# Kernel tuning notes

Measured on AMD Instinct MI355X. Metric: run time of the kernel, lower is better.

The kernel has to match this reference:

```python
import jax, jax.numpy as jnp
import numpy as np

# ---- config (mirrors the repo-level globals) ----
B, N = 8, 1024                 # batch, points per cloud
SHAPE_SIZE = 256               # per-point shape-code width
HEAD = 8                       # point_size + 1 - shape_size passthrough channels
SC_HID = 256                   # shape_code_encoder_hidden_dims = [256]
SC_OUT = 128                   # shape_code_encoder_output_size
E = 16                         # num_categories
INTER = HEAD + SC_OUT          # 136
ENC_DIMS = [INTER, 256, 512]   # encoder_hidden_dims
LATENT = 1024                  # latent_size
DEC_DIMS = [LATENT, 1024, 2048]
MAX_PTS, PSI = 1024, 7         # max_num_points, point_size_intermediate
DEC_OUT = (PSI + 1) * MAX_PTS  # 8192


def setup_inputs() -> dict:
    key = jax.random.key(0)
    ks = jax.random.split(key, 20)
    s = 0.02
    inp = {
        'x': jax.random.normal(ks[0], (B, HEAD + SHAPE_SIZE, N), jnp.float32),
        'cats': jax.random.randint(ks[1], (B, N), 0, E),
        # per-category shape encoders: Linear(256->256) ReLU Linear(256->128)
        'W1': jax.random.normal(ks[2], (E, SHAPE_SIZE, SC_HID), jnp.float32) * s,
        'b1': jnp.zeros((E, SC_HID), jnp.float32),
        'W2': jax.random.normal(ks[3], (E, SC_HID, SC_OUT), jnp.float32) * s,
        'b2': jnp.zeros((E, SC_OUT), jnp.float32),
        # pointwise Conv1d stack 136->256->512->1024 (weights [out,in])
        'Wc1': jax.random.normal(ks[4], (ENC_DIMS[1], ENC_DIMS[0]), jnp.float32) * s,
        'bc1': jnp.zeros((ENC_DIMS[1],), jnp.float32),
        'Wc2': jax.random.normal(ks[5], (ENC_DIMS[2], ENC_DIMS[1]), jnp.float32) * s,
        'bc2': jnp.zeros((ENC_DIMS[2],), jnp.float32),
        'Wc3': jax.random.normal(ks[6], (LATENT, ENC_DIMS[2]), jnp.float32) * s,
        'bc3': jnp.zeros((LATENT,), jnp.float32),
        # decoder MLP 1024->1024->2048->8192 (weights [in,out])
        'Wd1': jax.random.normal(ks[7], (DEC_DIMS[0], DEC_DIMS[1]), jnp.float32) * s,
        'bd1': jnp.zeros((DEC_DIMS[1],), jnp.float32),
        'Wd2': jax.random.normal(ks[8], (DEC_DIMS[1], DEC_DIMS[2]), jnp.float32) * s,
        'bd2': jnp.zeros((DEC_DIMS[2],), jnp.float32),
        'Wd3': jax.random.normal(ks[9], (DEC_DIMS[2], DEC_OUT), jnp.float32) * s,
        'bd3': jnp.zeros((DEC_OUT,), jnp.float32),
    }
    return inp


def reference(x, cats, W1, b1, W2, b2, Wc1, bc1, Wc2, bc2, Wc3, bc3,
              Wd1, bd1, Wd2, bd2, Wd3, bd3):
    # ---- encoder: category-routed per-point shape MLP ----
    sf = jnp.swapaxes(x[:, -SHAPE_SIZE:, :], 1, 2)      # [B, N, 256]
    mask = jax.nn.one_hot(cats, E, dtype=x.dtype)       # [B, N, E]
    routed = jnp.zeros((B, N, SC_OUT), x.dtype)
    for e in range(E):  # fixed small expert loop; avoids [B,N,E,hid] blowup
        h = jax.nn.relu(sf @ W1[e] + b1[e])             # [B, N, 256]
        o = h @ W2[e] + b2[e]                           # [B, N, 128]
        routed = routed + mask[..., e:e + 1] * o
    xi = jnp.concatenate([x[:, :HEAD, :], jnp.swapaxes(routed, 1, 2)], axis=1)  # [B,136,N]
    # ---- pointwise conv stack + max pool ----
    h = jax.nn.relu(jnp.einsum('oc,bcn->bon', Wc1, xi) + bc1[:, None])
    h = jax.nn.relu(jnp.einsum('oc,bcn->bon', Wc2, h) + bc2[:, None])
    h = jnp.einsum('oc,bcn->bon', Wc3, h) + bc3[:, None]  # [B, 1024, N]
    latent = jnp.max(h, axis=2)                            # [B, 1024]
    # ---- decoder MLP ----
    d = jax.nn.relu(latent @ Wd1 + bd1)
    d = jax.nn.relu(d @ Wd2 + bd2)
    out = (d @ Wd3 + bd3).reshape(B, MAX_PTS, PSI + 1)     # [B, 1024, 8]
    return out, latent
```

## Files before the change

kernel.cpp:

```cpp
#include <hip/hip_runtime.h>
#include <math.h>

#define BB 8
#define NN 1024
#define HEADC 8
#define SS 256
#define SCO 128
#define NE 16
#define C1 256
#define C2 512
#define C3 1024
#define NPTS (BB*NN)
#define XCH (HEADC+SS)
#define K1P 192
#define BK 64

typedef unsigned short ushortT;
typedef __attribute__((ext_vector_type(8))) short bf16x8;
typedef __attribute__((ext_vector_type(4))) float f32x4;

#define OB_XTB    0ull
#define OB_HB     4325376ull
#define OB_H2     0ull
#define OB_XI     8519680ull
#define OB_H1     11665408ull
#define OB_WT1    15859712ull
#define OB_WT2    15958016ull
#define OB_WT3    16220160ull
#define OB_W1T    17268736ull
#define OB_W2T    19365888ull
#define OB_PMAX   20414464ull
#define OB_LAT    20676608ull
#define OB_D1     20709376ull
#define OB_D2     20742144ull
#define OB_DPARTA 20807680ull
#define OB_DPARTB 22904832ull
#define OB_DPARTC 20807680ull
#define OB_IDX    33390592ull
#define OB_OFFS   33423360ull

__device__ __forceinline__ ushortT f2b(float f) {
  unsigned u = __float_as_uint(f);
  return (ushortT)((u + 0x7FFFu + ((u >> 16) & 1u)) >> 16);
}

#define CW_S1 (256*192)
#define CW_S2 (512*256)
#define CW_S3 (1024*512)
#define PREP_P1 2304
#define PREP_P2 5056
#define PREP_P3 7104
#define PREP_GRID 7105

__global__ __launch_bounds__(256) void k_prep_all(
    const float* __restrict__ x, ushortT* __restrict__ xTb, ushortT* __restrict__ xi,
    const float* __restrict__ Wc1, const float* __restrict__ Wc2,
    const float* __restrict__ Wc3, ushortT* __restrict__ w1c,
    ushortT* __restrict__ w2c, ushortT* __restrict__ w3c,
    const float* __restrict__ W1, const float* __restrict__ W2,
    ushortT* __restrict__ W1tb, ushortT* __restrict__ W2tb,
    const int* __restrict__ cats, int* __restrict__ idx, int* __restrict__ offs) {
  __shared__ float t[32][33];
  __shared__ int cnt[NE], base[NE + 1], cur[NE];
  int bid = blockIdx.x;
  int tid = threadIdx.x;

  if (bid < PREP_P1) {
    int bx = bid & 31, by = (bid >> 5) % 9, bz = bid / 288;
    int n0 = bx * 32, c0 = by * 32;
    int tx = tid & 31, ty = tid >> 5;
    const float* s = x + (size_t)bz * XCH * NN;
    for (int yy = ty; yy < 32; yy += 8) {
      int c = c0 + yy;
      if (c < XCH) t[yy][tx] = s[(size_t)c * NN + n0 + tx];
    }
    __syncthreads();
    for (int yy = ty; yy < 32; yy += 8) {
      int n = n0 + yy, c = c0 + tx;
      if (c < XCH) {
        ushortT v = f2b(t[tx][yy]);
        xTb[(size_t)(bz * NN + n) * XCH + c] = v;
        if (c < HEADC) xi[(size_t)(bz * NN + n) * K1P + c] = v;
      }
    }
  } else if (bid < PREP_P2) {
    int i = (bid - PREP_P1) * 256 + tid;
    if (i < CW_S1) {
      int r = i / K1P, c = i - r * K1P;
      w1c[i] = (c < 136) ? f2b(Wc1[(size_t)r * 136 + c]) : (ushortT)0;
    } else if (i < CW_S1 + CW_S2) {
      int k = i - CW_S1;
      w2c[k] = f2b(Wc2[k]);
    } else if (i < CW_S1 + CW_S2 + CW_S3) {
      int k = i - CW_S1 - CW_S2;
      w3c[k] = f2b(Wc3[k]);
    }
  } else if (bid < PREP_P3) {
    int tt = bid - PREP_P2;
    int z = tt >> 6, ry = (tt >> 3) & 7, cx = tt & 7;
    const float* s;
    ushortT* d;
    int C;
    if (z < 16) { s = W1 + (size_t)z * 65536; d = W1tb + (size_t)z * 65536; C = 256; }
    else {
      if (cx >= 4) return;
      s = W2 + (size_t)(z - 16) * 32768; d = W2tb + (size_t)(z - 16) * 32768; C = 128;
    }
    int r0 = ry * 32, c0 = cx * 32;
    int tx = tid & 31, ty = tid >> 5;
    for (int yy = ty; yy < 32; yy += 8) {
      int r = r0 + yy, c = c0 + tx;
      if (c < C) t[yy][tx] = s[(size_t)r * C + c];
    }
    __syncthreads();
    for (int yy = ty; yy < 32; yy += 8) {
      int c = c0 + yy, r = r0 + tx;
      if (c < C) d[(size_t)c * 256 + r] = f2b(t[tx][yy]);
    }
  } else {
    if (tid < NE) cnt[tid] = 0;
    __syncthreads();
    for (int p = tid; p < NPTS; p += 256) atomicAdd(&cnt[cats[p]], 1);
    __syncthreads();
    if (tid == 0) {
      int s = 0;
      for (int e = 0; e < NE; ++e) { base[e] = s; cur[e] = s; s += cnt[e]; }
      base[NE] = s;
    }
    __syncthreads();
    for (int p = tid; p < NPTS; p += 256) {
      int pos = atomicAdd(&cur[cats[p]], 1);
      idx[pos] = p;
    }
    if (tid <= NE) offs[tid] = base[tid];
  }
}

template<int MODE>
__global__ __launch_bounds__(256) void k_gemm(
    const ushortT* __restrict__ A, int lda,
    const ushortT* __restrict__ Bt, int ldb,
    const float* __restrict__ bias,
    ushortT* __restrict__ Cb, int ldc,
    float* __restrict__ pmaxOut,
    const int* __restrict__ idx, const int* __restrict__ offsp,
    int K, int relu) {
  __shared__ ushortT As[128 * BK];
  __shared__ ushortT Bs[128 * BK];
  __shared__ int pts[128];
  __shared__ float smax[2][128];
  int tid = threadIdx.x;
  int wave = tid >> 6, lane = tid & 63;
  int wm = wave >> 1, wn = wave & 1;
  int g = lane >> 4, lr = lane & 15;
  int n0 = blockIdx.x * 128;
  int m0 = 0, nr = 128, bucket0 = 0;

  if constexpr (MODE == 2 || MODE == 3) {
    int e = blockIdx.y, t = blockIdx.z;
    int s0 = offsp[e];
    int cnt = offsp[e + 1] - s0;
    int p0 = t * 128;
    if (p0 >= cnt) return;
    nr = min(128, cnt - p0);
    bucket0 = s0 + p0;
    Bt += (size_t)e * ((MODE == 2) ? 256 * 256 : 128 * 256);
    bias += e * ((MODE == 2) ? 256 : 128);
    if (tid < 128) pts[tid] = (tid < nr) ? idx[bucket0 + tid] : 0;
  } else {
    m0 = blockIdx.y * 128;
  }

  f32x4 acc[4][4];
#pragma unroll
  for (int mi = 0; mi < 4; ++mi)
#pragma unroll
    for (int nj = 0; nj < 4; ++nj) acc[mi][nj] = (f32x4)(0.f);

  int nkt = K / BK;
  for (int kt = 0; kt < nkt; ++kt) {
    int k0 = kt * BK;
    __syncthreads();
#pragma unroll
    for (int i = 0; i < 4; ++i) {
      int c = tid + i * 256;
      int row = c >> 3, slot = c & 7;
      int ss = slot ^ (row & 7);
      uint4 v;
      if constexpr (MODE == 2) {
        if (row < nr) v = *(const uint4*)(A + (size_t)pts[row] * lda + 8 + k0 + slot * 8);
        else { v.x = v.y = v.z = v.w = 0u; }
      } else if constexpr (MODE == 3) {
        if (row < nr) v = *(const uint4*)(A + (size_t)(bucket0 + row) * lda + k0 + slot * 8);
        else { v.x = v.y = v.z = v.w = 0u; }
      } else {
        v = *(const uint4*)(A + (size_t)(m0 + row) * lda + k0 + slot * 8);
      }
      *(uint4*)(As + row * BK + ss * 8) = v;
      uint4 w = *(const uint4*)(Bt + (size_t)(n0 + row) * ldb + k0 + slot * 8);
      *(uint4*)(Bs + row * BK + ss * 8) = w;
    }
    __syncthreads();
#pragma unroll
    for (int kk = 0; kk < 2; ++kk) {
      bf16x8 av[4], bv[4];
#pragma unroll
      for (int mi = 0; mi < 4; ++mi) {
        int row = wm * 64 + mi * 16 + lr;
        int slot = (kk * 4 + g) ^ (row & 7);
        av[mi] = *(const bf16x8*)(As + row * BK + slot * 8);
      }
#pragma unroll
      for (int nj = 0; nj < 4; ++nj) {
        int row = wn * 64 + nj * 16 + lr;
        int slot = (kk * 4 + g) ^ (row & 7);
        bv[nj] = *(const bf16x8*)(Bs + row * BK + slot * 8);
      }
#pragma unroll
      for (int mi = 0; mi < 4; ++mi)
#pragma unroll
        for (int nj = 0; nj < 4; ++nj)
          acc[mi][nj] = __builtin_amdgcn_mfma_f32_16x16x32_bf16(av[mi], bv[nj], acc[mi][nj], 0, 0, 0);
    }
  }

  if constexpr (MODE == 1) {
#pragma unroll
    for (int nj = 0; nj < 4; ++nj) {
      float m = -INFINITY;
#pragma unroll
      for (int mi = 0; mi < 4; ++mi)
#pragma unroll
        for (int r = 0; r < 4; ++r) m = fmaxf(m, acc[mi][nj][r]);
      m = fmaxf(m, __shfl_xor(m, 16));
      m = fmaxf(m, __shfl_xor(m, 32));
      if (lane < 16) smax[wm][wn * 64 + nj * 16 + lr] = m;
    }
    __syncthreads();
    if (tid < 128) {
      float m = fmaxf(smax[0][tid], smax[1][tid]);
      pmaxOut[(size_t)blockIdx.y * C3 + n0 + tid] = m + bias[n0 + tid];
    }
  } else {
#pragma unroll
    for (int mi = 0; mi < 4; ++mi)
#pragma unroll
      for (int nj = 0; nj < 4; ++nj)
#pragma unroll
        for (int r = 0; r < 4; ++r) {
          int lrow = wm * 64 + mi * 16 + g * 4 + r;
          int col = n0 + wn * 64 + nj * 16 + lr;
          float v = acc[mi][nj][r] + bias[col];
          if (relu) v = fmaxf(v, 0.f);
          ushortT b = f2b(v);
          if constexpr (MODE == 0) {
            Cb[(size_t)(m0 + lrow) * ldc + col] = b;
          } else if constexpr (MODE == 2) {
            if (lrow < nr) Cb[(size_t)(bucket0 + lrow) * ldc + col] = b;
          } else {
            if (lrow < nr) Cb[(size_t)pts[lrow] * ldc + 8 + col] = b;
          }
        }
  }
}

__global__ __launch_bounds__(256) void k_latmax(
    const float* __restrict__ pmax, float* __restrict__ lat, float* __restrict__ outLat) {
  int id4 = blockIdx.x * 256 + threadIdx.x;
  int b = id4 >> 8, o4 = id4 & 255;
  f32x4 m = (f32x4)(-INFINITY);
  for (int t = 0; t < 8; ++t) {
    f32x4 v = *(const f32x4*)(pmax + (size_t)((b << 3) + t) * C3 + o4 * 4);
#pragma unroll
    for (int r = 0; r < 4; ++r) m[r] = fmaxf(m[r], v[r]);
  }
  *(f32x4*)(lat + (size_t)id4 * 4) = m;
  *(f32x4*)(outLat + (size_t)id4 * 4) = m;
}

template<int CHUNKLOG, int T>
__global__ __launch_bounds__(T, 1) void k_dec(
    const float* __restrict__ A, const float* __restrict__ W,
    float* __restrict__ part, int K, int N) {
  constexpr int CHUNK = 1 << CHUNKLOG;
  __shared__ float a[8 << CHUNKLOG];
  int i0 = blockIdx.y << CHUNKLOG;
  int tid = threadIdx.x;
  for (int idx = tid; idx < (8 << CHUNKLOG); idx += T)
    a[idx] = A[(size_t)(idx >> CHUNKLOG) * K + i0 + (idx & (CHUNK - 1))];
  __syncthreads();

  int col = (blockIdx.x * T + tid) * 4;
  const float* wp = W + (size_t)i0 * N + col;
  f32x4 acc[8];
#pragma unroll
  for (int r = 0; r < 8; ++r) acc[r] = (f32x4)(0.f);

  f32x4 wa[8], wb[8];
#pragma unroll
  for (int q = 0; q < 8; ++q) wa[q] = *(const f32x4*)(wp + (size_t)q * N);
#pragma unroll
  for (int q = 0; q < 8; ++q) wb[q] = *(const f32x4*)(wp + (size_t)(8 + q) * N);

  for (int k0 = 0; k0 < CHUNK; k0 += 16) {
#pragma unroll
    for (int r = 0; r < 8; ++r) {
      f32x4 av0 = *(const f32x4*)(&a[(r << CHUNKLOG) + k0]);
      f32x4 av1 = *(const f32x4*)(&a[(r << CHUNKLOG) + k0 + 4]);
      acc[r] += av0[0] * wa[0] + av0[1] * wa[1] + av0[2] * wa[2] + av0[3] * wa[3];
      acc[r] += av1[0] * wa[4] + av1[1] * wa[5] + av1[2] * wa[6] + av1[3] * wa[7];
    }
    if (k0 + 16 < CHUNK) {
#pragma unroll
      for (int q = 0; q < 8; ++q) wa[q] = *(const f32x4*)(wp + (size_t)(k0 + 16 + q) * N);
    }
#pragma unroll
    for (int r = 0; r < 8; ++r) {
      f32x4 av0 = *(const f32x4*)(&a[(r << CHUNKLOG) + k0 + 8]);
      f32x4 av1 = *(const f32x4*)(&a[(r << CHUNKLOG) + k0 + 12]);
      acc[r] += av0[0] * wb[0] + av0[1] * wb[1] + av0[2] * wb[2] + av0[3] * wb[3];
      acc[r] += av1[0] * wb[4] + av1[1] * wb[5] + av1[2] * wb[6] + av1[3] * wb[7];
    }
    if (k0 + 24 < CHUNK) {
#pragma unroll
      for (int q = 0; q < 8; ++q) wb[q] = *(const f32x4*)(wp + (size_t)(k0 + 24 + q) * N);
    }
  }

  float* pp = part + (size_t)(blockIdx.y * 8) * N + col;
#pragma unroll
  for (int r = 0; r < 8; ++r) *(f32x4*)(pp + (size_t)r * N) = acc[r];
}

__global__ __launch_bounds__(256) void k_reduce4(
    const float* __restrict__ part, const float* __restrict__ bias,
    float* __restrict__ out, int N, int KC, int doRelu) {
  int o4 = blockIdx.x * 256 + threadIdx.x;
  int col4 = o4 & ((N >> 2) - 1);
  f32x4 s = ((const f32x4*)bias)[col4];
  const f32x4* p4 = (const f32x4*)part;
#pragma unroll 8
  for (int kc = 0; kc < KC; ++kc)
    s += p4[(size_t)kc * 2 * N + o4];
  if (doRelu) {
#pragma unroll
    for (int r = 0; r < 4; ++r) s[r] = fmaxf(s[r], 0.f);
  }
  ((f32x4*)out)[o4] = s;
}

extern "C" void kernel_launch(void* const* d_in, const int* in_sizes, int n_in,
                              void* d_out, int out_size, void* d_ws, size_t ws_size,
                              hipStream_t stream) {
  const float* x    = (const float*)d_in[0];
  const int*   cats = (const int*)d_in[1];
  const float* W1   = (const float*)d_in[2];
  const float* b1   = (const float*)d_in[3];
  const float* W2   = (const float*)d_in[4];
  const float* b2   = (const float*)d_in[5];
  const float* Wc1  = (const float*)d_in[6];
  const float* bc1  = (const float*)d_in[7];
  const float* Wc2  = (const float*)d_in[8];
  const float* bc2  = (const float*)d_in[9];
  const float* Wc3  = (const float*)d_in[10];
  const float* bc3  = (const float*)d_in[11];
  const float* Wd1  = (const float*)d_in[12];
  const float* bd1  = (const float*)d_in[13];
  const float* Wd2  = (const float*)d_in[14];
  const float* bd2  = (const float*)d_in[15];
  const float* Wd3  = (const float*)d_in[16];
  const float* bd3  = (const float*)d_in[17];
  float* out = (float*)d_out;

  char* wsb = (char*)d_ws;
  ushortT* xTb  = (ushortT*)(wsb + OB_XTB);
  ushortT* hB   = (ushortT*)(wsb + OB_HB);
  ushortT* h2   = (ushortT*)(wsb + OB_H2);
  ushortT* xi   = (ushortT*)(wsb + OB_XI);
  ushortT* h1   = (ushortT*)(wsb + OB_H1);
  ushortT* Wt1b = (ushortT*)(wsb + OB_WT1);
  ushortT* Wt2b = (ushortT*)(wsb + OB_WT2);
  ushortT* Wt3b = (ushortT*)(wsb + OB_WT3);
  ushortT* W1tb = (ushortT*)(wsb + OB_W1T);
  ushortT* W2tb = (ushortT*)(wsb + OB_W2T);
  float* pmax   = (float*)(wsb + OB_PMAX);
  float* lat    = (float*)(wsb + OB_LAT);
  float* d1w    = (float*)(wsb + OB_D1);
  float* d2w    = (float*)(wsb + OB_D2);
  float* dpA    = (float*)(wsb + OB_DPARTA);
  float* dpB    = (float*)(wsb + OB_DPARTB);
  float* dpC    = (float*)(wsb + OB_DPARTC);
  int*   idx    = (int*)(wsb + OB_IDX);
  int*   offs   = (int*)(wsb + OB_OFFS);

  k_prep_all<<<PREP_GRID, 256, 0, stream>>>(
      x, xTb, xi, Wc1, Wc2, Wc3, Wt1b, Wt2b, Wt3b, W1, W2, W1tb, W2tb,
      cats, idx, offs);

  k_gemm<2><<<dim3(2, NE, 8), 256, 0, stream>>>(xTb, XCH, W1tb, 256, b1, hB, 256,
                                                nullptr, idx, offs, 256, 1);
  k_gemm<3><<<dim3(1, NE, 8), 256, 0, stream>>>(hB, 256, W2tb, 256, b2, xi, K1P,
                                                nullptr, idx, offs, 256, 0);

  k_gemm<0><<<dim3(2, 64), 256, 0, stream>>>(xi, K1P, Wt1b, K1P, bc1, h1, 256,
                                             nullptr, nullptr, nullptr, K1P, 1);
  k_gemm<0><<<dim3(4, 64), 256, 0, stream>>>(h1, 256, Wt2b, 256, bc2, h2, 512,
                                             nullptr, nullptr, nullptr, 256, 1);
  k_gemm<1><<<dim3(8, 64), 256, 0, stream>>>(h2, 512, Wt3b, 512, bc3, nullptr, 0,
                                             pmax, nullptr, nullptr, 512, 0);
  k_latmax<<<8, 256, 0, stream>>>(pmax, lat, out + 65536);

  k_dec<4, 128><<<dim3(2, 64), 128, 0, stream>>>(lat, Wd1, dpA, 1024, 1024);
  k_reduce4<<<8, 256, 0, stream>>>(dpA, bd1, d1w, 1024, 64, 1);
  k_dec<4, 128><<<dim3(4, 64), 128, 0, stream>>>(d1w, Wd2, dpB, 1024, 2048);
  k_reduce4<<<16, 256, 0, stream>>>(dpB, bd2, d2w, 2048, 64, 1);
  k_dec<6, 256><<<dim3(8, 32), 256, 0, stream>>>(d2w, Wd3, dpC, 2048, 8192);
  k_reduce4<<<64, 256, 0, stream>>>(dpC, bd3, out, 8192, 32, 0);
  (void)in_sizes; (void)n_in; (void)out_size; (void)ws_size;
}
```

Before: 270.8 us.

## Double-buffer GEMM tiles via direct global-to-LDS loads and fuse latent max into decoder

The bf16 MFMA GEMM now stages A/B tiles with global_load_lds into two LDS buffers, prefetching the next k-tile while computing the current one and using one barrier per iteration. The separate latent max-pool kernel is removed and its reduction is folded into the first decoder GEMV's activation load, which also writes the latent output. The decoder GEMV weight prefetch becomes a three-deep register rotation with a fully unrolled k loop. This adds LDS use and register pressure, and out-of-range rows in routed tiles now load unmasked data that is later discarded.

```diff
diff --git a/kernel.cpp b/kernel.cpp
--- a/kernel.cpp
+++ b/kernel.cpp
@@ -30,7 +30,6 @@
 #define OB_W1T    17268736ull
 #define OB_W2T    19365888ull
 #define OB_PMAX   20414464ull
-#define OB_LAT    20676608ull
 #define OB_D1     20709376ull
 #define OB_D2     20742144ull
 #define OB_DPARTA 20807680ull
@@ -42,6 +41,12 @@
 __device__ __forceinline__ ushortT f2b(float f) {
   unsigned u = __float_as_uint(f);
   return (ushortT)((u + 0x7FFFu + ((u >> 16) & 1u)) >> 16);
+}
+
+__device__ __forceinline__ void gl16(const void* g, void* l) {
+  __builtin_amdgcn_global_load_lds(
+      (const __attribute__((address_space(1))) unsigned int*)g,
+      (__attribute__((address_space(3))) unsigned int*)l, 16, 0, 0);
 }
 
 #define CW_S1 (256*192)
@@ -145,8 +150,8 @@
     float* __restrict__ pmaxOut,
     const int* __restrict__ idx, const int* __restrict__ offsp,
     int K, int relu) {
-  __shared__ ushortT As[128 * BK];
-  __shared__ ushortT Bs[128 * BK];
+  __shared__ ushortT As[2][128 * BK];
+  __shared__ ushortT Bs[2][128 * BK];
   __shared__ int pts[128];
   __shared__ float smax[2][128];
   int tid = threadIdx.x;
@@ -170,6 +175,29 @@
   } else {
     m0 = blockIdx.y * 128;
   }
+  __syncthreads();
+
+  auto stage = [&](int b, int kt) {
+    int k0 = kt * BK;
+#pragma unroll
+    for (int i = 0; i < 4; ++i) {
+      int cbase = i * 256 + wave * 64;
+      int c = cbase + lane;
+      int row = c >> 3, p = c & 7;
+      int sslot = p ^ (row & 7);
+      const ushortT* ga;
+      if constexpr (MODE == 2) {
+        ga = A + (size_t)pts[row] * lda + 8 + k0 + sslot * 8;
+      } else if constexpr (MODE == 3) {
+        ga = A + (size_t)(bucket0 + row) * lda + k0 + sslot * 8;
+      } else {
+        ga = A + (size_t)(m0 + row) * lda + k0 + sslot * 8;
+      }
+      gl16(ga, (void*)(As[b] + (size_t)cbase * 8));
+      gl16(Bt + (size_t)(n0 + row) * ldb + k0 + sslot * 8,
+           (void*)(Bs[b] + (size_t)cbase * 8));
+    }
+  };
 
   f32x4 acc[4][4];
 #pragma unroll
@@ -178,29 +206,11 @@
     for (int nj = 0; nj < 4; ++nj) acc[mi][nj] = (f32x4)(0.f);
 
   int nkt = K / BK;
+  stage(0, 0);
+  __syncthreads();
+  int buf = 0;
   for (int kt = 0; kt < nkt; ++kt) {
-    int k0 = kt * BK;
-    __syncthreads();
-#pragma unroll
-    for (int i = 0; i < 4; ++i) {
-      int c = tid + i * 256;
-      int row = c >> 3, slot = c & 7;
-      int ss = slot ^ (row & 7);
-      uint4 v;
-      if constexpr (MODE == 2) {
-        if (row < nr) v = *(const uint4*)(A + (size_t)pts[row] * lda + 8 + k0 + slot * 8);
-        else { v.x = v.y = v.z = v.w = 0u; }
-      } else if constexpr (MODE == 3) {
-        if (row < nr) v = *(const uint4*)(A + (size_t)(bucket0 + row) * lda + k0 + slot * 8);
-        else { v.x = v.y = v.z = v.w = 0u; }
-      } else {
-        v = *(const uint4*)(A + (size_t)(m0 + row) * lda + k0 + slot * 8);
-      }
-      *(uint4*)(As + row * BK + ss * 8) = v;
-      uint4 w = *(const uint4*)(Bt + (size_t)(n0 + row) * ldb + k0 + slot * 8);
-      *(uint4*)(Bs + row * BK + ss * 8) = w;
-    }
-    __syncthreads();
+    if (kt + 1 < nkt) stage(buf ^ 1, kt + 1);
 #pragma unroll
     for (int kk = 0; kk < 2; ++kk) {
       bf16x8 av[4], bv[4];
@@ -208,13 +218,13 @@
       for (int mi = 0; mi < 4; ++mi) {
         int row = wm * 64 + mi * 16 + lr;
         int slot = (kk * 4 + g) ^ (row & 7);
-        av[mi] = *(const bf16x8*)(As + row * BK + slot * 8);
+        av[mi] = *(const bf16x8*)(As[buf] + row * BK + slot * 8);
       }
 #pragma unroll
       for (int nj = 0; nj < 4; ++nj) {
         int row = wn * 64 + nj * 16 + lr;
         int slot = (kk * 4 + g) ^ (row & 7);
-        bv[nj] = *(const bf16x8*)(Bs + row * BK + slot * 8);
+        bv[nj] = *(const bf16x8*)(Bs[buf] + row * BK + slot * 8);
       }
 #pragma unroll
       for (int mi = 0; mi < 4; ++mi)
@@ -222,6 +232,8 @@
         for (int nj = 0; nj < 4; ++nj)
           acc[mi][nj] = __builtin_amdgcn_mfma_f32_16x16x32_bf16(av[mi], bv[nj], acc[mi][nj], 0, 0, 0);
     }
+    __syncthreads();
+    buf ^= 1;
   }
 
   if constexpr (MODE == 1) {
@@ -264,30 +276,29 @@
   }
 }
 
-__global__ __launch_bounds__(256) void k_latmax(
-    const float* __restrict__ pmax, float* __restrict__ lat, float* __restrict__ outLat) {
-  int id4 = blockIdx.x * 256 + threadIdx.x;
-  int b = id4 >> 8, o4 = id4 & 255;
-  f32x4 m = (f32x4)(-INFINITY);
-  for (int t = 0; t < 8; ++t) {
-    f32x4 v = *(const f32x4*)(pmax + (size_t)((b << 3) + t) * C3 + o4 * 4);
-#pragma unroll
-    for (int r = 0; r < 4; ++r) m[r] = fmaxf(m[r], v[r]);
-  }
-  *(f32x4*)(lat + (size_t)id4 * 4) = m;
-  *(f32x4*)(outLat + (size_t)id4 * 4) = m;
-}
-
-template<int CHUNKLOG, int T>
+template<int CHUNKLOG, int T, bool LMAX>
 __global__ __launch_bounds__(T, 1) void k_dec(
-    const float* __restrict__ A, const float* __restrict__ W,
-    float* __restrict__ part, int K, int N) {
+    const float* __restrict__ Asrc, const float* __restrict__ W,
+    float* __restrict__ part, float* __restrict__ outLat, int K, int N) {
   constexpr int CHUNK = 1 << CHUNKLOG;
+  constexpr int G = CHUNK / 8;
   __shared__ float a[8 << CHUNKLOG];
   int i0 = blockIdx.y << CHUNKLOG;
   int tid = threadIdx.x;
-  for (int idx = tid; idx < (8 << CHUNKLOG); idx += T)
-    a[idx] = A[(size_t)(idx >> CHUNKLOG) * K + i0 + (idx & (CHUNK - 1))];
+  for (int idx = tid; idx < (8 << CHUNKLOG); idx += T) {
+    int r = idx >> CHUNKLOG, i = idx & (CHUNK - 1);
+    float v;
+    if constexpr (LMAX) {
+      v = -INFINITY;
+#pragma unroll
+      for (int t = 0; t < 8; ++t)
+        v = fmaxf(v, Asrc[(size_t)((r << 3) + t) * K + i0 + i]);
+      if (blockIdx.x == 0) outLat[(size_t)r * K + i0 + i] = v;
+    } else {
+      v = Asrc[(size_t)r * K + i0 + i];
+    }
+    a[idx] = v;
+  }
   __syncthreads();
 
   int col = (blockIdx.x * T + tid) * 4;
@@ -296,34 +307,30 @@
 #pragma unroll
   for (int r = 0; r < 8; ++r) acc[r] = (f32x4)(0.f);
 
-  f32x4 wa[8], wb[8];
-#pragma unroll
-  for (int q = 0; q < 8; ++q) wa[q] = *(const f32x4*)(wp + (size_t)q * N);
-#pragma unroll
-  for (int q = 0; q < 8; ++q) wb[q] = *(const f32x4*)(wp + (size_t)(8 + q) * N);
-
-  for (int k0 = 0; k0 < CHUNK; k0 += 16) {
+  f32x4 wreg[3][8];
+#pragma unroll
+  for (int gg = 0; gg < (G < 3 ? G : 3); ++gg)
+#pragma unroll
+    for (int q = 0; q < 8; ++q)
+      wreg[gg][q] = *(const f32x4*)(wp + (size_t)(gg * 8 + q) * N);
+
+#pragma unroll
+  for (int gi = 0; gi < G; ++gi) {
+    constexpr int B3[8] = {0, 1, 2, 0, 1, 2, 0, 1};
+    const int b = B3[gi & 7];
 #pragma unroll
     for (int r = 0; r < 8; ++r) {
-      f32x4 av0 = *(const f32x4*)(&a[(r << CHUNKLOG) + k0]);
-      f32x4 av1 = *(const f32x4*)(&a[(r << CHUNKLOG) + k0 + 4]);
-      acc[r] += av0[0] * wa[0] + av0[1] * wa[1] + av0[2] * wa[2] + av0[3] * wa[3];
-      acc[r] += av1[0] * wa[4] + av1[1] * wa[5] + av1[2] * wa[6] + av1[3] * wa[7];
-    }
-    if (k0 + 16 < CHUNK) {
-#pragma unroll
-      for (int q = 0; q < 8; ++q) wa[q] = *(const f32x4*)(wp + (size_t)(k0 + 16 + q) * N);
-    }
-#pragma unroll
-    for (int r = 0; r < 8; ++r) {
-      f32x4 av0 = *(const f32x4*)(&a[(r << CHUNKLOG) + k0 + 8]);
-      f32x4 av1 = *(const f32x4*)(&a[(r << CHUNKLOG) + k0 + 12]);
-      acc[r] += av0[0] * wb[0] + av0[1] * wb[1] + av0[2] * wb[2] + av0[3] * wb[3];
-      acc[r] += av1[0] * wb[4] + av1[1] * wb[5] + av1[2] * wb[6] + av1[3] * wb[7];
-    }
-    if (k0 + 24 < CHUNK) {
-#pragma unroll
-      for (int q = 0; q < 8; ++q) wb[q] = *(const f32x4*)(wp + (size_t)(k0 + 24 + q) * N);
+      f32x4 av0 = *(const f32x4*)(&a[(r << CHUNKLOG) + gi * 8]);
+      f32x4 av1 = *(const f32x4*)(&a[(r << CHUNKLOG) + gi * 8 + 4]);
+      acc[r] += av0[0] * wreg[b][0] + av0[1] * wreg[b][1] +
+                av0[2] * wreg[b][2] + av0[3] * wreg[b][3];
+      acc[r] += av1[0] * wreg[b][4] + av1[1] * wreg[b][5] +
+                av1[2] * wreg[b][6] + av1[3] * wreg[b][7];
+    }
+    if (gi + 3 < G) {
+#pragma unroll
+      for (int q = 0; q < 8; ++q)
+        wreg[b][q] = *(const f32x4*)(wp + (size_t)((gi + 3) * 8 + q) * N);
     }
   }
 
@@ -384,7 +391,6 @@
   ushortT* W1tb = (ushortT*)(wsb + OB_W1T);
   ushortT* W2tb = (ushortT*)(wsb + OB_W2T);
   float* pmax   = (float*)(wsb + OB_PMAX);
-  float* lat    = (float*)(wsb + OB_LAT);
   float* d1w    = (float*)(wsb + OB_D1);
   float* d2w    = (float*)(wsb + OB_D2);
   float* dpA    = (float*)(wsb + OB_DPARTA);
@@ -408,13 +414,15 @@
                                              nullptr, nullptr, nullptr, 256, 1);
   k_gemm<1><<<dim3(8, 64), 256, 0, stream>>>(h2, 512, Wt3b, 512, bc3, nullptr, 0,
                                              pmax, nullptr, nullptr, 512, 0);
-  k_latmax<<<8, 256, 0, stream>>>(pmax, lat, out + 65536);
-
-  k_dec<4, 128><<<dim3(2, 64), 128, 0, stream>>>(lat, Wd1, dpA, 1024, 1024);
+
+  k_dec<4, 128, true><<<dim3(2, 64), 128, 0, stream>>>(pmax, Wd1, dpA,
+                                                       out + 65536, 1024, 1024);
   k_reduce4<<<8, 256, 0, stream>>>(dpA, bd1, d1w, 1024, 64, 1);
-  k_dec<4, 128><<<dim3(4, 64), 128, 0, stream>>>(d1w, Wd2, dpB, 1024, 2048);
+  k_dec<4, 128, false><<<dim3(4, 64), 128, 0, stream>>>(d1w, Wd2, dpB,
+                                                        nullptr, 1024, 2048);
   k_reduce4<<<16, 256, 0, stream>>>(dpB, bd2, d2w, 2048, 64, 1);
-  k_dec<6, 256><<<dim3(8, 32), 256, 0, stream>>>(d2w, Wd3, dpC, 2048, 8192);
+  k_dec<6, 256, false><<<dim3(8, 32), 256, 0, stream>>>(d2w, Wd3, dpC,
+                                                        nullptr, 2048, 8192);
   k_reduce4<<<64, 256, 0, stream>>>(dpC, bd3, out, 8192, 32, 0);
   (void)in_sizes; (void)n_in; (void)out_size; (void)ws_size;
 }
```

After: 273.9 us. No clear change (+1.1%).
